# Kernel optimization log

Measured on AMD Instinct MI355X. Metric: run time of the kernel, lower is better.

The kernel has to match this reference:

```python
import jax, jax.numpy as jnp
import numpy as np

GAMMA_EXP = 1.0 / 2.2
PATTERN = 'RGGB'
H, W = 3072, 4096


def _conv1d(x, k, axis):
    """Cross-correlation of 2D x with 1D kernel k along axis, reflect padding
    (matches torch F.conv2d on reflect-padded input)."""
    p = (len(k) - 1) // 2
    pad = [(p, p) if a == axis else (0, 0) for a in range(2)]
    xp = jnp.pad(x, pad, mode='reflect')
    n = x.shape[axis]
    out = jnp.zeros_like(x)
    for i, ki in enumerate(k):
        if ki == 0.0:
            continue
        sl = [slice(None), slice(None)]
        sl[axis] = slice(i, i + n)
        out = out + ki * xp[tuple(sl)]
    return out


def _bayer_masks(shape, pattern):
    ch = {c: np.zeros((2, 2), np.float32) for c in 'RGB'}
    for i, c in enumerate(pattern):
        ch[c][i // 2, i % 2] = 1.0
    reps = ((shape[0] + 1) // 2, (shape[1] + 1) // 2)
    return tuple(jnp.asarray(np.tile(ch[c], reps)[:shape[0], :shape[1]]) for c in 'RGB')


def _shift_left2(x, axis):
    # pad by 2 on the far side with reflect, then drop first 2 -> x[j+2] with reflect at border
    pad = [(0, 2) if a == axis else (0, 0) for a in range(2)]
    xp = jnp.pad(x, pad, mode='reflect')
    sl = [slice(None), slice(None)]
    sl[axis] = slice(2, None)
    return xp[tuple(sl)]


def _menon2007(CFA, pattern):
    R_m, G_m, B_m = _bayer_masks(CFA.shape, pattern)
    h0 = [0.0, 0.5, 0.0, 0.5, 0.0]
    h1 = [-0.25, 0.0, 0.5, 0.0, -0.25]

    R = CFA * R_m
    G = CFA * G_m
    B = CFA * B_m

    G_H = jnp.where(G_m == 0, _conv1d(CFA, h0, 1) + _conv1d(CFA, h1, 1), G)
    G_V = jnp.where(G_m == 0, _conv1d(CFA, h0, 0) + _conv1d(CFA, h1, 0), G)

    C_H = jnp.where(R_m == 1, R - G_H, 0.0)
    C_H = jnp.where(B_m == 1, B - G_H, C_H)
    C_V = jnp.where(R_m == 1, R - G_V, 0.0)
    C_V = jnp.where(B_m == 1, B - G_V, C_V)

    D_H = jnp.abs(C_H - _shift_left2(C_H, axis=1))
    D_V = jnp.abs(C_V - _shift_left2(C_V, axis=0))

    k_row = [0.0, 0.0, 3.0, 0.0, 3.0]   # k[2, :]
    k_col = [1.0, 0.0, 3.0, 0.0, 1.0]   # k[:, 2]
    d_H = _conv1d(D_H, k_row, 1) + _conv1d(D_H, k_col, 0) - D_H * 3.0
    d_V = _conv1d(D_V, k_row, 1) + _conv1d(D_V, k_col, 0) - D_V * 3.0

    M = (d_V >= d_H).astype(CFA.dtype)
    G = jnp.where(G_m == 1, G, M * G_H + (1.0 - M) * G_V)

    R_r = jnp.any(R_m == 1, axis=1, keepdims=True) & jnp.ones_like(R_m, bool)
    B_r = jnp.any(B_m == 1, axis=1, keepdims=True) & jnp.ones_like(B_m, bool)
    kb = [0.5, 0.0, 0.5]

    R = jnp.where((G_m == 1) & R_r, G + _conv1d(R, kb, 1) - _conv1d(G, kb, 1), R)
    R = jnp.where((G_m == 1) & B_r, G + _conv1d(R, kb, 0) - _conv1d(G, kb, 0), R)
    B = jnp.where((G_m == 1) & B_r, G + _conv1d(B, kb, 1) - _conv1d(G, kb, 1), B)
    B = jnp.where((G_m == 1) & R_r, G + _conv1d(B, kb, 0) - _conv1d(G, kb, 0), B)

    R_at_B = M * (B + _conv1d(R, kb, 1) - _conv1d(B, kb, 1)) \
           + (1.0 - M) * (B + _conv1d(R, kb, 0) - _conv1d(B, kb, 0))
    R = jnp.where(B_r & (B_m == 1), R_at_B, R)

    B_at_R = M * (R + _conv1d(B, kb, 1) - _conv1d(R, kb, 1)) \
           + (1.0 - M) * (R + _conv1d(B, kb, 0) - _conv1d(R, kb, 0))
    B = jnp.where(R_r & (R_m == 1), B_at_R, B)

    return jnp.stack([R, G, B], axis=0)


def setup_inputs() -> dict:
    key = jax.random.key(0)
    k1, _ = jax.random.split(key)
    raw = jax.random.uniform(k1, (H, W), dtype=jnp.float32)
    wb = jnp.array([1.6, 1.2, 1.4], dtype=jnp.float32).reshape(3, 1, 1)
    return {"raw": raw, "wb": wb}


def reference(raw, wb):
    scaled = raw.astype(jnp.float32) / 65535.0
    rgb = _menon2007(scaled, PATTERN)
    rgb = rgb * wb
    rgb = jnp.clip(rgb, 0.0, 1.0)
    mn = jnp.min(rgb)
    mx = jnp.max(rgb)
    rng = mx - mn
    rgb = jnp.where(rng > 1e-6, (rgb - mn) / jnp.maximum(rng, 1e-12), rgb)
    rgb = jnp.power(jnp.maximum(rgb, 1e-12), GAMMA_EXP)
    return rgb
```

## Files before the change

kernel.cpp:

```cpp
#include <hip/hip_runtime.h>
#include <hip/hip_bf16.h>
#include <hip/hip_fp16.h>

#pragma clang fp contract(off)

constexpr int IMG_H = 3072;
constexpr int IMG_W = 4096;
constexpr int TS = 32;
constexpr float GAMMA_E = (float)(1.0 / 2.2);
constexpr float SC = 1048576.0f;
constexpr float INV_SC = 1.0f / SC;

__device__ __forceinline__ int mir(int v, int n) {
    v = (v < 0) ? -v : v;
    return (v >= n) ? (2 * n - 2 - v) : v;
}

constexpr int OFF_CFA = 0;               constexpr int CFA_STR = 45;
constexpr int OFF_GH  = OFF_CFA + 46*45; constexpr int GH_STR  = 41;
constexpr int OFF_GV  = OFF_GH  + 40*41; constexpr int GV_STR  = 39;
constexpr int OFF_DH  = OFF_GV  + 42*39; constexpr int DH_STR  = 39;
constexpr int OFF_DV  = OFF_DH  + 40*39; constexpr int DV_STR  = 39;
constexpr int OFF_G   = OFF_DV  + 40*39; constexpr int G_STR   = 37;
constexpr int SMEM_N  = OFF_G   + 36*37;
constexpr int OFF_HH  = OFF_DH;          constexpr int HV_STR  = 35;
constexpr int OFF_VV  = OFF_DV;

__global__ void init_slots(unsigned int* slots) {
    int t = threadIdx.x;
    if (t < 512) slots[t] = (t < 256) ? 0x7F800000u : 0u;
}

__device__ __forceinline__ float pack_gm(float g, unsigned mb) {
    return __uint_as_float((__float_as_uint(g) & ~1u) | mb);
}

template <bool FP16>
__global__ __launch_bounds__(256) void demosaic_pass1(
    const float* __restrict__ raw, const float* __restrict__ wb,
    float* __restrict__ out, __half* __restrict__ hout,
    unsigned int* __restrict__ slots)
{
    __shared__ float sm[SMEM_N];
    __shared__ float redmn[4], redmx[4];
    const int tid = threadIdx.x;
    const int tx = tid & 31, ty = tid >> 5;
    const int gr0 = blockIdx.y * TS;
    const int gc0 = blockIdx.x * TS;
    const bool fast = (blockIdx.x != 0) && (blockIdx.x != gridDim.x - 1) &&
                      (blockIdx.y != 0) && (blockIdx.y != gridDim.y - 1);

    if (fast) {
        const float* src = raw + (long long)(gr0 - 6) * IMG_W + (gc0 - 4);
        for (int i = tid; i < 46 * 11; i += 256) {
            int ar = i / 11, ic = (i % 11) << 2;
            float4 v = *(const float4*)(src + ar * IMG_W + ic);
            int b = OFF_CFA + ar * CFA_STR + ic;
            sm[b + 0] = v.x / 65535.0f; sm[b + 1] = v.y / 65535.0f;
            sm[b + 2] = v.z / 65535.0f; sm[b + 3] = v.w / 65535.0f;
        }
        __syncthreads();

        auto doGH = [&](int ar, int ac) {
            int cb = OFF_CFA + (ar + 2) * CFA_STR + (ac + 2);
            float x0 = sm[cb];
            float t0 = 0.5f * sm[cb - 1] + 0.5f * sm[cb + 1];
            float t1 = (-0.25f * sm[cb - 2] + 0.5f * x0) + (-0.25f * sm[cb + 2]);
            sm[OFF_GH + ar * GH_STR + ac] = ((ar + ac) & 1) ? x0 : (t0 + t1);
        };
        auto doGV = [&](int ar, int ac) {
            int cb = OFF_CFA + (ar + 2) * CFA_STR + (ac + 2);
            float x0 = sm[cb];
            float t0 = 0.5f * sm[cb - CFA_STR] + 0.5f * sm[cb + CFA_STR];
            float t1 = (-0.25f * sm[cb - 2 * CFA_STR] + 0.5f * x0) + (-0.25f * sm[cb + 2 * CFA_STR]);
            sm[OFF_GV + ar * GV_STR + ac] = ((ar + ac) & 1) ? x0 : (t0 + t1);
        };
#pragma unroll
        for (int r0 = 0; r0 < 5; ++r0) {
            int ar = ty + r0 * 8;
            doGH(ar, tx);
            if (tx < 8) doGH(ar, tx + 32);
        }
#pragma unroll
        for (int r0 = 0; r0 < 6; ++r0) {
            int ar = ty + r0 * 8;
            if (ar < 42) {
                doGV(ar, tx);
                if (tx < 6) doGV(ar, tx + 32);
            }
        }
        __syncthreads();

        auto doD = [&](int ar, int ac) {
            int cb = OFF_CFA + (ar + 2) * CFA_STR + (ac + 2);
            float c00 = sm[cb];
            float aH = c00 - sm[OFF_GH + ar * GH_STR + ac];
            float bH = sm[cb + 2] - sm[OFF_GH + ar * GH_STR + (ac + 2)];
            float aV = c00 - sm[OFF_GV + ar * GV_STR + ac];
            float bV = sm[cb + 2 * CFA_STR] - sm[OFF_GV + (ar + 2) * GV_STR + ac];
            sm[OFF_DH + ar * DH_STR + ac] = fabsf(aH - bH);
            sm[OFF_DV + ar * DV_STR + ac] = fabsf(aV - bV);
        };
#pragma unroll
        for (int r0 = 0; r0 < 5; ++r0) {
            int ar = ty + r0 * 8;
            doD(ar, tx);
            if (tx < 6) doD(ar, tx + 32);
        }
        __syncthreads();

        auto doMG = [&](int ar, int ac) {
            int db = OFF_DH + (ar + 2) * DH_STR + ac;
            float Dh0 = sm[db];
            float trowH = 3.0f * Dh0 + 3.0f * sm[db + 2];
            float tcolH = (sm[db - 2 * DH_STR] + 3.0f * Dh0) + sm[db + 2 * DH_STR];
            float dHv = (trowH + tcolH) - 3.0f * Dh0;
            int vb = OFF_DV + (ar + 2) * DV_STR + ac;
            float Dv0 = sm[vb];
            float trowV = 3.0f * Dv0 + 3.0f * sm[vb + 2];
            float tcolV = (sm[vb - 2 * DV_STR] + 3.0f * Dv0) + sm[vb + 2 * DV_STR];
            float dVv = (trowV + tcolV) - 3.0f * Dv0;
            unsigned mb = (dVv >= dHv) ? 1u : 0u;
            float g = ((ar + ac) & 1) ? sm[OFF_CFA + (ar + 4) * CFA_STR + (ac + 2)]
                     : (mb ? sm[OFF_GH + (ar + 2) * GH_STR + ac]
                           : sm[OFF_GV + (ar + 2) * GV_STR + ac]);
            sm[OFF_G + ar * G_STR + ac] = pack_gm(g, mb);
        };
#pragma unroll
        for (int r0 = 0; r0 < 5; ++r0) {
            int ar = ty + r0 * 8;
            if (ar < 36) {
                doMG(ar, tx);
                if (tx < 4) doMG(ar, tx + 32);
            }
        }
        __syncthreads();

        auto doHV = [&](int ar, int ac) {
            int gb = OFF_G + (ar + 1) * G_STR + (ac + 1);
            int cb = OFF_CFA + (ar + 5) * CFA_STR + (ac + 3);
            float g0 = sm[gb];
            float hh = g0 + 0.5f * (sm[cb - 1] + sm[cb + 1] - sm[gb - 1] - sm[gb + 1]);
            float vv = g0 + 0.5f * (sm[cb - CFA_STR] + sm[cb + CFA_STR] - sm[gb - G_STR] - sm[gb + G_STR]);
            sm[OFF_HH + ar * HV_STR + ac] = hh;
            sm[OFF_VV + ar * HV_STR + ac] = vv;
        };
#pragma unroll
        for (int r0 = 0; r0 < 5; ++r0) {
            int ar = ty + r0 * 8;
            if (ar < 34) {
                doHV(ar, tx);
                if (tx < 2) doHV(ar, tx + 32);
            }
        }
    } else {
        auto CFA = [&](int r, int c) -> float { return sm[OFF_CFA + (r - gr0 + 6) * CFA_STR + (c - gc0 + 4)]; };
        auto GH  = [&](int r, int c) -> float { return sm[OFF_GH  + (r - gr0 + 4) * GH_STR  + (c - gc0 + 2)]; };
        auto GV  = [&](int r, int c) -> float { return sm[OFF_GV  + (r - gr0 + 4) * GV_STR  + (c - gc0 + 2)]; };
        auto DH  = [&](int r, int c) -> float { return sm[OFF_DH  + (r - gr0 + 4) * DH_STR  + (c - gc0 + 2)]; };
        auto DV  = [&](int r, int c) -> float { return sm[OFF_DV  + (r - gr0 + 4) * DV_STR  + (c - gc0 + 2)]; };
        auto Gg  = [&](int r, int c) -> float { return sm[OFF_G   + (r - gr0 + 2) * G_STR   + (c - gc0 + 2)]; };

        for (int i = tid; i < 46 * 44; i += 256) {
            int ar = i / 44, ac = i % 44;
            int r2 = mir(gr0 + ar - 6, IMG_H), c2 = mir(gc0 + ac - 4, IMG_W);
            sm[OFF_CFA + ar * CFA_STR + ac] = raw[r2 * IMG_W + c2] / 65535.0f;
        }
        __syncthreads();
        for (int i = tid; i < 40 * 40; i += 256) {
            int ar = i / 40, ac = i % 40;
            int r2 = mir(gr0 + ar - 4, IMG_H), c2 = mir(gc0 + ac - 2, IMG_W);
            float x0 = CFA(r2, c2);
            float t0 = 0.5f * CFA(r2, c2 - 1) + 0.5f * CFA(r2, c2 + 1);
            float t1 = (-0.25f * CFA(r2, c2 - 2) + 0.5f * x0) + (-0.25f * CFA(r2, c2 + 2));
            sm[OFF_GH + ar * GH_STR + ac] = (((r2 + c2) & 1) ? x0 : (t0 + t1));
        }
        for (int i = tid; i < 42 * 38; i += 256) {
            int ar = i / 38, ac = i % 38;
            int r2 = mir(gr0 + ar - 4, IMG_H), c2 = mir(gc0 + ac - 2, IMG_W);
            float x0 = CFA(r2, c2);
            float t0 = 0.5f * CFA(r2 - 1, c2) + 0.5f * CFA(r2 + 1, c2);
            float t1 = (-0.25f * CFA(r2 - 2, c2) + 0.5f * x0) + (-0.25f * CFA(r2 + 2, c2));
            sm[OFF_GV + ar * GV_STR + ac] = (((r2 + c2) & 1) ? x0 : (t0 + t1));
        }
        __syncthreads();
        for (int i = tid; i < 40 * 38; i += 256) {
            int ar = i / 38, ac = i % 38;
            int r2 = mir(gr0 + ar - 4, IMG_H), c2 = mir(gc0 + ac - 2, IMG_W);
            float aH = CFA(r2, c2) - GH(r2, c2);
            float bH = CFA(r2, c2 + 2) - GH(r2, c2 + 2);
            float aV = CFA(r2, c2) - GV(r2, c2);
            float bV = CFA(r2 + 2, c2) - GV(r2 + 2, c2);
            sm[OFF_DH + ar * DH_STR + ac] = fabsf(aH - bH);
            sm[OFF_DV + ar * DV_STR + ac] = fabsf(aV - bV);
        }
        __syncthreads();
        for (int i = tid; i < 36 * 36; i += 256) {
            int ar = i / 36, ac = i % 36;
            int r2 = mir(gr0 + ar - 2, IMG_H), c2 = mir(gc0 + ac - 2, IMG_W);
            float Dh0 = DH(r2, c2);
            float trowH = 3.0f * Dh0 + 3.0f * DH(r2, c2 + 2);
            float tcolH = (DH(r2 - 2, c2) + 3.0f * Dh0) + DH(r2 + 2, c2);
            float dHv = (trowH + tcolH) - 3.0f * Dh0;
            float Dv0 = DV(r2, c2);
            float trowV = 3.0f * Dv0 + 3.0f * DV(r2, c2 + 2);
            float tcolV = (DV(r2 - 2, c2) + 3.0f * Dv0) + DV(r2 + 2, c2);
            float dVv = (trowV + tcolV) - 3.0f * Dv0;
            unsigned mb = (dVv >= dHv) ? 1u : 0u;
            float g = ((r2 + c2) & 1) ? CFA(r2, c2) : (mb ? GH(r2, c2) : GV(r2, c2));
            sm[OFF_G + ar * G_STR + ac] = pack_gm(g, mb);
        }
        __syncthreads();
        for (int i = tid; i < 34 * 34; i += 256) {
            int ar = i / 34, ac = i % 34;
            int r2 = mir(gr0 + ar - 1, IMG_H), c2 = mir(gc0 + ac - 1, IMG_W);
            float g0 = Gg(r2, c2);
            float hh = g0 + 0.5f * (CFA(r2, c2 - 1) + CFA(r2, c2 + 1) - Gg(r2, c2 - 1) - Gg(r2, c2 + 1));
            float vv = g0 + 0.5f * (CFA(r2 - 1, c2) + CFA(r2 + 1, c2) - Gg(r2 - 1, c2) - Gg(r2 + 1, c2));
            sm[OFF_HH + ar * HV_STR + ac] = hh;
            sm[OFF_VV + ar * HV_STR + ac] = vv;
        }
    }
    __syncthreads();

    const float wr = wb[0], wg = wb[1], wbv = wb[2];
    const int pr = tid >> 3;
    const int pc0 = (tid & 7) << 2;
    const bool rowOdd = (pr & 1) != 0;
    float mn = 1e30f, mx = -1e30f;
    float rr[4], gg[4], bb[4];
    __half hr[4], hg[4], hb[4];
#pragma unroll
    for (int d = 0; d < 4; ++d) {
        const int pc = pc0 + d;
        const int hhb = OFF_HH + (pr + 1) * HV_STR + (pc + 1);
        const int vvb = OFF_VV + (pr + 1) * HV_STR + (pc + 1);
        const float cfa = sm[OFF_CFA + (pr + 6) * CFA_STR + (pc + 4)];
        const float g = sm[OFF_G + (pr + 2) * G_STR + (pc + 2)];
        const unsigned mb = __float_as_uint(g) & 1u;
        float sH = (sm[hhb - 1] - sm[vvb - 1]) + (sm[hhb + 1] - sm[vvb + 1]);
        float sV = (sm[hhb - HV_STR] - sm[vvb - HV_STR]) + (sm[hhb + HV_STR] - sm[vvb + HV_STR]);
        float X = mb ? (cfa - 0.5f * sH) : (cfa + 0.5f * sV);
        float R, B;
        if ((d & 1) == 0) {
            R = rowOdd ? sm[vvb] : cfa;
            B = rowOdd ? sm[hhb] : X;
        } else {
            R = rowOdd ? X : sm[hhb];
            B = rowOdd ? cfa : sm[vvb];
        }
        R = fminf(fmaxf(R * wr, 0.f), 1.f);
        float Gx = fminf(fmaxf(g * wg, 0.f), 1.f);
        B = fminf(fmaxf(B * wbv, 0.f), 1.f);
        if constexpr (FP16) {
            hr[d] = __float2half(R * SC);  R  = __half2float(hr[d]);
            hg[d] = __float2half(Gx * SC); Gx = __half2float(hg[d]);
            hb[d] = __float2half(B * SC);  B  = __half2float(hb[d]);
        }
        mn = fminf(mn, fminf(R, fminf(Gx, B)));
        mx = fmaxf(mx, fmaxf(R, fmaxf(Gx, B)));
        rr[d] = R; gg[d] = Gx; bb[d] = B;
    }
    const long long HW = (long long)IMG_H * IMG_W;
    const long long base = (long long)(gr0 + pr) * IMG_W + (gc0 + pc0);
    if constexpr (FP16) {
        auto pack = [](__half a, __half b) {
            __half2 p = __halves2half2(a, b);
            return *reinterpret_cast<unsigned int*>(&p);
        };
        uint2 ur = make_uint2(pack(hr[0], hr[1]), pack(hr[2], hr[3]));
        uint2 ug = make_uint2(pack(hg[0], hg[1]), pack(hg[2], hg[3]));
        uint2 ub = make_uint2(pack(hb[0], hb[1]), pack(hb[2], hb[3]));
        *(uint2*)(hout + base)          = ur;
        *(uint2*)(hout + HW + base)     = ug;
        *(uint2*)(hout + 2 * HW + base) = ub;
    } else {
        *(float4*)(out + base)          = make_float4(rr[0], rr[1], rr[2], rr[3]);
        *(float4*)(out + HW + base)     = make_float4(gg[0], gg[1], gg[2], gg[3]);
        *(float4*)(out + 2 * HW + base) = make_float4(bb[0], bb[1], bb[2], bb[3]);
    }

#pragma unroll
    for (int off2 = 32; off2 > 0; off2 >>= 1) {
        mn = fminf(mn, __shfl_xor(mn, off2));
        mx = fmaxf(mx, __shfl_xor(mx, off2));
    }
    if ((tid & 63) == 0) { redmn[tid >> 6] = mn; redmx[tid >> 6] = mx; }
    __syncthreads();
    if (tid == 0) {
        mn = fminf(fminf(redmn[0], redmn[1]), fminf(redmn[2], redmn[3]));
        mx = fmaxf(fmaxf(redmx[0], redmx[1]), fmaxf(redmx[2], redmx[3]));
        if constexpr (FP16) { mn *= INV_SC; mx *= INV_SC; }
        int slot = (int)((blockIdx.y * gridDim.x + blockIdx.x) & 255);
        atomicMin(&slots[slot], __float_as_uint(mn));
        atomicMax(&slots[256 + slot], __float_as_uint(mx));
    }
}

__device__ __forceinline__ void reduce_slots(const unsigned int* slots, int tid,
                                             float* smn, float* smx, float& mn, float& mx) {
    mn = __uint_as_float(slots[tid]);
    mx = __uint_as_float(slots[256 + tid]);
#pragma unroll
    for (int off2 = 32; off2 > 0; off2 >>= 1) {
        mn = fminf(mn, __shfl_xor(mn, off2));
        mx = fmaxf(mx, __shfl_xor(mx, off2));
    }
    if ((tid & 63) == 0) { smn[tid >> 6] = mn; smx[tid >> 6] = mx; }
    __syncthreads();
    mn = fminf(fminf(smn[0], smn[1]), fminf(smn[2], smn[3]));
    mx = fmaxf(fmaxf(smx[0], smx[1]), fmaxf(smx[2], smx[3]));
}

__device__ __forceinline__ float gamma_hw(float a) {
    return __builtin_amdgcn_exp2f(GAMMA_E * __builtin_amdgcn_logf(a));
}

__global__ __launch_bounds__(256) void finalize_pass2_h(
    const __half* __restrict__ hin, float* __restrict__ out,
    const unsigned int* __restrict__ slots)
{
    __shared__ float smn[4], smx[4];
    const int tid = threadIdx.x;
    float mn, mx;
    reduce_slots(slots, tid, smn, smx, mn, mx);
    const float rng = mx - mn;
    const bool app = rng > 1e-6f;
    const float invden = 1.0f / fmaxf(rng, 1e-12f);

    const long long n8 = (long long)3 * IMG_H * IMG_W / 8;
    const uint4* pin = (const uint4*)hin;
    float4* po = (float4*)out;
    for (long long idx = (long long)blockIdx.x * blockDim.x + tid; idx < n8;
         idx += (long long)gridDim.x * blockDim.x) {
        uint4 u = pin[idx];
        float f[8];
        float2 t;
        t = __half22float2(*(__half2*)&u.x); f[0] = t.x; f[1] = t.y;
        t = __half22float2(*(__half2*)&u.y); f[2] = t.x; f[3] = t.y;
        t = __half22float2(*(__half2*)&u.z); f[4] = t.x; f[5] = t.y;
        t = __half22float2(*(__half2*)&u.w); f[6] = t.x; f[7] = t.y;
#pragma unroll
        for (int k = 0; k < 8; ++k) {
            float a = f[k] * INV_SC;
            a = app ? (a - mn) * invden : a;
            f[k] = gamma_hw(fmaxf(a, 1e-12f));
        }
        po[2 * idx]     = make_float4(f[0], f[1], f[2], f[3]);
        po[2 * idx + 1] = make_float4(f[4], f[5], f[6], f[7]);
    }
}

__global__ __launch_bounds__(256) void finalize_pass2_f(
    float* __restrict__ out, const unsigned int* __restrict__ slots)
{
    __shared__ float smn[4], smx[4];
    const int tid = threadIdx.x;
    float mn, mx;
    reduce_slots(slots, tid, smn, smx, mn, mx);
    const float rng = mx - mn;
    const bool app = rng > 1e-6f;
    const float invden = 1.0f / fmaxf(rng, 1e-12f);

    const long long n4 = (long long)3 * IMG_H * IMG_W / 4;
    float4* p = (float4*)out;
    for (long long idx = (long long)blockIdx.x * blockDim.x + tid; idx < n4;
         idx += (long long)gridDim.x * blockDim.x) {
        float4 v = p[idx];
        v.x = gamma_hw(fmaxf(app ? (v.x - mn) * invden : v.x, 1e-12f));
        v.y = gamma_hw(fmaxf(app ? (v.y - mn) * invden : v.y, 1e-12f));
        v.z = gamma_hw(fmaxf(app ? (v.z - mn) * invden : v.z, 1e-12f));
        v.w = gamma_hw(fmaxf(app ? (v.w - mn) * invden : v.w, 1e-12f));
        p[idx] = v;
    }
}

extern "C" void kernel_launch(void* const* d_in, const int* in_sizes, int n_in,
                              void* d_out, int out_size, void* d_ws, size_t ws_size,
                              hipStream_t stream) {
    (void)in_sizes; (void)n_in; (void)out_size;
    const float* raw = (const float*)d_in[0];
    const float* wb = (const float*)d_in[1];
    float* out = (float*)d_out;
    unsigned int* slots = (unsigned int*)d_ws;
    __half* hplanes = (__half*)((char*)d_ws + 4096);
    const size_t need = 4096 + (size_t)3 * IMG_H * IMG_W * sizeof(__half);
    const bool use_fp16 = ws_size >= need;

    init_slots<<<1, 512, 0, stream>>>(slots);
    dim3 grid(IMG_W / TS, IMG_H / TS);
    if (use_fp16) {
        demosaic_pass1<true><<<grid, 256, 0, stream>>>(raw, wb, out, hplanes, slots);
        finalize_pass2_h<<<dim3(2048), 256, 0, stream>>>(hplanes, out, slots);
    } else {
        demosaic_pass1<false><<<grid, 256, 0, stream>>>(raw, wb, out, hplanes, slots);
        finalize_pass2_f<<<dim3(2048), 256, 0, stream>>>(out, slots);
    }
}
```

Baseline: 170.6 us.

## Vectorize shared-memory stencil stages with aligned strides and float4 register windows

Changes all shared-memory tile strides to multiples of four and aligns the buffer. Each thread now processes four adjacent outputs per stage, loading sliding windows with float4/float2 LDS accesses and reusing them in registers, both in the interior fast path and the final output stage. This cuts LDS instruction count but gives up the odd padding strides, so bank conflicts may return and register pressure rises; the GV stage uses column-blocked register tiles.

Result: faster. 165.4 us (-3.1%).

```diff
diff --git a/kernel.cpp b/kernel.cpp
--- a/kernel.cpp
+++ b/kernel.cpp
@@ -16,14 +16,16 @@
     return (v >= n) ? (2 * n - 2 - v) : v;
 }
 
-constexpr int OFF_CFA = 0;               constexpr int CFA_STR = 45;
-constexpr int OFF_GH  = OFF_CFA + 46*45; constexpr int GH_STR  = 41;
-constexpr int OFF_GV  = OFF_GH  + 40*41; constexpr int GV_STR  = 39;
-constexpr int OFF_DH  = OFF_GV  + 42*39; constexpr int DH_STR  = 39;
-constexpr int OFF_DV  = OFF_DH  + 40*39; constexpr int DV_STR  = 39;
-constexpr int OFF_G   = OFF_DV  + 40*39; constexpr int G_STR   = 37;
-constexpr int SMEM_N  = OFF_G   + 36*37;
-constexpr int OFF_HH  = OFF_DH;          constexpr int HV_STR  = 35;
+constexpr int CFA_STR = 44, GH_STR = 40, GV_STR = 40, DH_STR = 40, DV_STR = 40,
+              G_STR = 36, HV_STR = 36;
+constexpr int OFF_CFA = 0;
+constexpr int OFF_GH  = OFF_CFA + 46*44;
+constexpr int OFF_GV  = OFF_GH  + 40*40;
+constexpr int OFF_DH  = OFF_GV  + 42*40;
+constexpr int OFF_DV  = OFF_DH  + 40*40;
+constexpr int OFF_G   = OFF_DV  + 40*40;
+constexpr int SMEM_N  = OFF_G   + 36*36;
+constexpr int OFF_HH  = OFF_DH;
 constexpr int OFF_VV  = OFF_DV;
 
 __global__ void init_slots(unsigned int* slots) {
@@ -41,10 +43,9 @@
     float* __restrict__ out, __half* __restrict__ hout,
     unsigned int* __restrict__ slots)
 {
-    __shared__ float sm[SMEM_N];
+    __shared__ __align__(16) float sm[SMEM_N];
     __shared__ float redmn[4], redmx[4];
     const int tid = threadIdx.x;
-    const int tx = tid & 31, ty = tid >> 5;
     const int gr0 = blockIdx.y * TS;
     const int gc0 = blockIdx.x * TS;
     const bool fast = (blockIdx.x != 0) && (blockIdx.x != gridDim.x - 1) &&
@@ -55,103 +56,161 @@
         for (int i = tid; i < 46 * 11; i += 256) {
             int ar = i / 11, ic = (i % 11) << 2;
             float4 v = *(const float4*)(src + ar * IMG_W + ic);
-            int b = OFF_CFA + ar * CFA_STR + ic;
-            sm[b + 0] = v.x / 65535.0f; sm[b + 1] = v.y / 65535.0f;
-            sm[b + 2] = v.z / 65535.0f; sm[b + 3] = v.w / 65535.0f;
-        }
-        __syncthreads();
-
-        auto doGH = [&](int ar, int ac) {
-            int cb = OFF_CFA + (ar + 2) * CFA_STR + (ac + 2);
-            float x0 = sm[cb];
-            float t0 = 0.5f * sm[cb - 1] + 0.5f * sm[cb + 1];
-            float t1 = (-0.25f * sm[cb - 2] + 0.5f * x0) + (-0.25f * sm[cb + 2]);
-            sm[OFF_GH + ar * GH_STR + ac] = ((ar + ac) & 1) ? x0 : (t0 + t1);
-        };
-        auto doGV = [&](int ar, int ac) {
-            int cb = OFF_CFA + (ar + 2) * CFA_STR + (ac + 2);
-            float x0 = sm[cb];
-            float t0 = 0.5f * sm[cb - CFA_STR] + 0.5f * sm[cb + CFA_STR];
-            float t1 = (-0.25f * sm[cb - 2 * CFA_STR] + 0.5f * x0) + (-0.25f * sm[cb + 2 * CFA_STR]);
-            sm[OFF_GV + ar * GV_STR + ac] = ((ar + ac) & 1) ? x0 : (t0 + t1);
-        };
-#pragma unroll
-        for (int r0 = 0; r0 < 5; ++r0) {
-            int ar = ty + r0 * 8;
-            doGH(ar, tx);
-            if (tx < 8) doGH(ar, tx + 32);
-        }
-#pragma unroll
-        for (int r0 = 0; r0 < 6; ++r0) {
-            int ar = ty + r0 * 8;
-            if (ar < 42) {
-                doGV(ar, tx);
-                if (tx < 6) doGV(ar, tx + 32);
-            }
-        }
-        __syncthreads();
-
-        auto doD = [&](int ar, int ac) {
-            int cb = OFF_CFA + (ar + 2) * CFA_STR + (ac + 2);
-            float c00 = sm[cb];
-            float aH = c00 - sm[OFF_GH + ar * GH_STR + ac];
-            float bH = sm[cb + 2] - sm[OFF_GH + ar * GH_STR + (ac + 2)];
-            float aV = c00 - sm[OFF_GV + ar * GV_STR + ac];
-            float bV = sm[cb + 2 * CFA_STR] - sm[OFF_GV + (ar + 2) * GV_STR + ac];
-            sm[OFF_DH + ar * DH_STR + ac] = fabsf(aH - bH);
-            sm[OFF_DV + ar * DV_STR + ac] = fabsf(aV - bV);
-        };
-#pragma unroll
-        for (int r0 = 0; r0 < 5; ++r0) {
-            int ar = ty + r0 * 8;
-            doD(ar, tx);
-            if (tx < 6) doD(ar, tx + 32);
-        }
-        __syncthreads();
-
-        auto doMG = [&](int ar, int ac) {
-            int db = OFF_DH + (ar + 2) * DH_STR + ac;
-            float Dh0 = sm[db];
-            float trowH = 3.0f * Dh0 + 3.0f * sm[db + 2];
-            float tcolH = (sm[db - 2 * DH_STR] + 3.0f * Dh0) + sm[db + 2 * DH_STR];
-            float dHv = (trowH + tcolH) - 3.0f * Dh0;
-            int vb = OFF_DV + (ar + 2) * DV_STR + ac;
-            float Dv0 = sm[vb];
-            float trowV = 3.0f * Dv0 + 3.0f * sm[vb + 2];
-            float tcolV = (sm[vb - 2 * DV_STR] + 3.0f * Dv0) + sm[vb + 2 * DV_STR];
-            float dVv = (trowV + tcolV) - 3.0f * Dv0;
-            unsigned mb = (dVv >= dHv) ? 1u : 0u;
-            float g = ((ar + ac) & 1) ? sm[OFF_CFA + (ar + 4) * CFA_STR + (ac + 2)]
-                     : (mb ? sm[OFF_GH + (ar + 2) * GH_STR + ac]
-                           : sm[OFF_GV + (ar + 2) * GV_STR + ac]);
-            sm[OFF_G + ar * G_STR + ac] = pack_gm(g, mb);
-        };
-#pragma unroll
-        for (int r0 = 0; r0 < 5; ++r0) {
-            int ar = ty + r0 * 8;
-            if (ar < 36) {
-                doMG(ar, tx);
-                if (tx < 4) doMG(ar, tx + 32);
-            }
-        }
-        __syncthreads();
-
-        auto doHV = [&](int ar, int ac) {
-            int gb = OFF_G + (ar + 1) * G_STR + (ac + 1);
-            int cb = OFF_CFA + (ar + 5) * CFA_STR + (ac + 3);
-            float g0 = sm[gb];
-            float hh = g0 + 0.5f * (sm[cb - 1] + sm[cb + 1] - sm[gb - 1] - sm[gb + 1]);
-            float vv = g0 + 0.5f * (sm[cb - CFA_STR] + sm[cb + CFA_STR] - sm[gb - G_STR] - sm[gb + G_STR]);
-            sm[OFF_HH + ar * HV_STR + ac] = hh;
-            sm[OFF_VV + ar * HV_STR + ac] = vv;
-        };
-#pragma unroll
-        for (int r0 = 0; r0 < 5; ++r0) {
-            int ar = ty + r0 * 8;
-            if (ar < 34) {
-                doHV(ar, tx);
-                if (tx < 2) doHV(ar, tx + 32);
-            }
+            *(float4*)&sm[OFF_CFA + ar * CFA_STR + ic] =
+                make_float4(v.x / 65535.0f, v.y / 65535.0f, v.z / 65535.0f, v.w / 65535.0f);
+        }
+        __syncthreads();
+
+        for (int i = tid; i < 400; i += 256) {
+            int ar = i / 10, ac4 = (i % 10) << 2;
+            int cb = OFF_CFA + (ar + 2) * CFA_STR + ac4;
+            const float4 a = *(const float4*)&sm[cb];
+            const float4 b = *(const float4*)&sm[cb + 4];
+            float w[8] = {a.x, a.y, a.z, a.w, b.x, b.y, b.z, b.w};
+            float o[4];
+#pragma unroll
+            for (int j = 0; j < 4; ++j) {
+                float x0 = w[j + 2];
+                float t0 = 0.5f * w[j + 1] + 0.5f * w[j + 3];
+                float t1 = (-0.25f * w[j] + 0.5f * x0) + (-0.25f * w[j + 4]);
+                o[j] = ((ar + ac4 + j) & 1) ? x0 : (t0 + t1);
+            }
+            *(float4*)&sm[OFF_GH + ar * GH_STR + ac4] = make_float4(o[0], o[1], o[2], o[3]);
+        }
+        if (tid < 110) {
+            int rg = tid / 10, ac4 = (tid % 10) << 2;
+            int r0 = (rg == 10) ? 38 : (rg << 2);
+            float c[4][8];
+#pragma unroll
+            for (int k = 0; k < 8; ++k) {
+                int rb = OFF_CFA + (r0 + k) * CFA_STR + ac4;
+                float2 p = *(const float2*)&sm[rb + 2];
+                float2 q = *(const float2*)&sm[rb + 4];
+                c[0][k] = p.x; c[1][k] = p.y; c[2][k] = q.x; c[3][k] = q.y;
+            }
+#pragma unroll
+            for (int ii = 0; ii < 4; ++ii) {
+                float o[4];
+#pragma unroll
+                for (int j = 0; j < 4; ++j) {
+                    float x0 = c[j][ii + 2];
+                    float t0 = 0.5f * c[j][ii + 1] + 0.5f * c[j][ii + 3];
+                    float t1 = (-0.25f * c[j][ii] + 0.5f * x0) + (-0.25f * c[j][ii + 4]);
+                    o[j] = ((r0 + ii + ac4 + j) & 1) ? x0 : (t0 + t1);
+                }
+                *(float4*)&sm[OFF_GV + (r0 + ii) * GV_STR + ac4] = make_float4(o[0], o[1], o[2], o[3]);
+            }
+        }
+        __syncthreads();
+
+        for (int i = tid; i < 400; i += 256) {
+            int ar = i / 10, ac4 = (i % 10) << 2;
+            int cb = OFF_CFA + (ar + 2) * CFA_STR + ac4;
+            const float4 a = *(const float4*)&sm[cb];
+            const float4 b = *(const float4*)&sm[cb + 4];
+            float cw[8] = {a.x, a.y, a.z, a.w, b.x, b.y, b.z, b.w};
+            float2 d0 = *(const float2*)&sm[OFF_CFA + (ar + 4) * CFA_STR + ac4 + 2];
+            float2 d1 = *(const float2*)&sm[OFF_CFA + (ar + 4) * CFA_STR + ac4 + 4];
+            float cd[4] = {d0.x, d0.y, d1.x, d1.y};
+            const float4 g0 = *(const float4*)&sm[OFF_GH + ar * GH_STR + ac4];
+            const float4 g1 = *(const float4*)&sm[OFF_GH + ar * GH_STR + ac4 + 4];
+            float gh[8] = {g0.x, g0.y, g0.z, g0.w, g1.x, g1.y, g1.z, g1.w};
+            const float4 v0 = *(const float4*)&sm[OFF_GV + ar * GV_STR + ac4];
+            const float4 v2 = *(const float4*)&sm[OFF_GV + (ar + 2) * GV_STR + ac4];
+            float gva[4] = {v0.x, v0.y, v0.z, v0.w};
+            float gvb[4] = {v2.x, v2.y, v2.z, v2.w};
+            float oh[4], ov[4];
+#pragma unroll
+            for (int j = 0; j < 4; ++j) {
+                float aH = cw[j + 2] - gh[j];
+                float bH = cw[j + 4] - gh[j + 2];
+                oh[j] = fabsf(aH - bH);
+                float aV = cw[j + 2] - gva[j];
+                float bV = cd[j] - gvb[j];
+                ov[j] = fabsf(aV - bV);
+            }
+            *(float4*)&sm[OFF_DH + ar * DH_STR + ac4] = make_float4(oh[0], oh[1], oh[2], oh[3]);
+            *(float4*)&sm[OFF_DV + ar * DV_STR + ac4] = make_float4(ov[0], ov[1], ov[2], ov[3]);
+        }
+        __syncthreads();
+
+        for (int i = tid; i < 324; i += 256) {
+            int ar = i / 9, ac4 = (i % 9) << 2;
+            int hb2 = OFF_DH + (ar + 2) * DH_STR + ac4;
+            const float4 h0 = *(const float4*)&sm[hb2];
+            const float4 h1 = *(const float4*)&sm[hb2 + 4];
+            float hw[8] = {h0.x, h0.y, h0.z, h0.w, h1.x, h1.y, h1.z, h1.w};
+            const float4 huq = *(const float4*)&sm[OFF_DH + ar * DH_STR + ac4];
+            const float4 hdq = *(const float4*)&sm[OFF_DH + (ar + 4) * DH_STR + ac4];
+            float hu[4] = {huq.x, huq.y, huq.z, huq.w};
+            float hd[4] = {hdq.x, hdq.y, hdq.z, hdq.w};
+            int vb2 = OFF_DV + (ar + 2) * DV_STR + ac4;
+            const float4 w0 = *(const float4*)&sm[vb2];
+            const float4 w1 = *(const float4*)&sm[vb2 + 4];
+            float vw[8] = {w0.x, w0.y, w0.z, w0.w, w1.x, w1.y, w1.z, w1.w};
+            const float4 vuq = *(const float4*)&sm[OFF_DV + ar * DV_STR + ac4];
+            const float4 vdq = *(const float4*)&sm[OFF_DV + (ar + 4) * DV_STR + ac4];
+            float vu[4] = {vuq.x, vuq.y, vuq.z, vuq.w};
+            float vd[4] = {vdq.x, vdq.y, vdq.z, vdq.w};
+            float2 c0 = *(const float2*)&sm[OFF_CFA + (ar + 4) * CFA_STR + ac4 + 2];
+            float2 c1 = *(const float2*)&sm[OFF_CFA + (ar + 4) * CFA_STR + ac4 + 4];
+            float cf[4] = {c0.x, c0.y, c1.x, c1.y};
+            const float4 ghq = *(const float4*)&sm[OFF_GH + (ar + 2) * GH_STR + ac4];
+            const float4 gvq = *(const float4*)&sm[OFF_GV + (ar + 2) * GV_STR + ac4];
+            float gha[4] = {ghq.x, ghq.y, ghq.z, ghq.w};
+            float gvv[4] = {gvq.x, gvq.y, gvq.z, gvq.w};
+            float o[4];
+#pragma unroll
+            for (int j = 0; j < 4; ++j) {
+                float Dh0 = hw[j];
+                float trowH = 3.0f * Dh0 + 3.0f * hw[j + 2];
+                float tcolH = (hu[j] + 3.0f * Dh0) + hd[j];
+                float dHv = (trowH + tcolH) - 3.0f * Dh0;
+                float Dv0 = vw[j];
+                float trowV = 3.0f * Dv0 + 3.0f * vw[j + 2];
+                float tcolV = (vu[j] + 3.0f * Dv0) + vd[j];
+                float dVv = (trowV + tcolV) - 3.0f * Dv0;
+                unsigned mb = (dVv >= dHv) ? 1u : 0u;
+                float g = ((ar + ac4 + j) & 1) ? cf[j] : (mb ? gha[j] : gvv[j]);
+                o[j] = pack_gm(g, mb);
+            }
+            *(float4*)&sm[OFF_G + ar * G_STR + ac4] = make_float4(o[0], o[1], o[2], o[3]);
+        }
+        __syncthreads();
+
+        for (int i = tid; i < 306; i += 256) {
+            int ar = i / 9, ac4 = (i % 9) << 2;
+            int gb1 = OFF_G + (ar + 1) * G_STR + ac4;
+            const float4 ga = *(const float4*)&sm[gb1];
+            const float4 gb2 = *(const float4*)&sm[gb1 + 4];
+            float gw[8] = {ga.x, ga.y, ga.z, ga.w, gb2.x, gb2.y, gb2.z, gb2.w};
+            const float4 guq = *(const float4*)&sm[OFF_G + ar * G_STR + ac4];
+            const float2 guq2 = *(const float2*)&sm[OFF_G + ar * G_STR + ac4 + 4];
+            float gu[6] = {guq.x, guq.y, guq.z, guq.w, guq2.x, guq2.y};
+            const float4 gdq = *(const float4*)&sm[OFF_G + (ar + 2) * G_STR + ac4];
+            const float2 gdq2 = *(const float2*)&sm[OFF_G + (ar + 2) * G_STR + ac4 + 4];
+            float gd[6] = {gdq.x, gdq.y, gdq.z, gdq.w, gdq2.x, gdq2.y};
+            int c5 = OFF_CFA + (ar + 5) * CFA_STR + ac4;
+            const float4 ca = *(const float4*)&sm[c5];
+            const float4 cb2 = *(const float4*)&sm[c5 + 4];
+            float cw[8] = {ca.x, ca.y, ca.z, ca.w, cb2.x, cb2.y, cb2.z, cb2.w};
+            int c4i = OFF_CFA + (ar + 4) * CFA_STR + ac4;
+            const float4 cua = *(const float4*)&sm[c4i];
+            const float4 cub = *(const float4*)&sm[c4i + 4];
+            float cu[8] = {cua.x, cua.y, cua.z, cua.w, cub.x, cub.y, cub.z, cub.w};
+            int c6i = OFF_CFA + (ar + 6) * CFA_STR + ac4;
+            const float4 cda = *(const float4*)&sm[c6i];
+            const float4 cdb = *(const float4*)&sm[c6i + 4];
+            float cdn[8] = {cda.x, cda.y, cda.z, cda.w, cdb.x, cdb.y, cdb.z, cdb.w};
+            float oh[4], ov[4];
+#pragma unroll
+            for (int j = 0; j < 4; ++j) {
+                float g0 = gw[j + 1];
+                oh[j] = g0 + 0.5f * (cw[j + 2] + cw[j + 4] - gw[j] - gw[j + 2]);
+                ov[j] = g0 + 0.5f * (cu[j + 3] + cdn[j + 3] - gu[j + 1] - gd[j + 1]);
+            }
+            *(float4*)&sm[OFF_HH + ar * HV_STR + ac4] = make_float4(oh[0], oh[1], oh[2], oh[3]);
+            *(float4*)&sm[OFF_VV + ar * HV_STR + ac4] = make_float4(ov[0], ov[1], ov[2], ov[3]);
         }
     } else {
         auto CFA = [&](int r, int c) -> float { return sm[OFF_CFA + (r - gr0 + 6) * CFA_STR + (c - gc0 + 4)]; };
@@ -227,39 +286,62 @@
     const int pr = tid >> 3;
     const int pc0 = (tid & 7) << 2;
     const bool rowOdd = (pr & 1) != 0;
+    int hbase = OFF_HH + (pr + 1) * HV_STR + pc0;
+    const float4 h1a = *(const float4*)&sm[hbase];
+    const float4 h1b = *(const float4*)&sm[hbase + 4];
+    float hwc[8] = {h1a.x, h1a.y, h1a.z, h1a.w, h1b.x, h1b.y, h1b.z, h1b.w};
+    int vbase = OFF_VV + (pr + 1) * HV_STR + pc0;
+    const float4 v1a = *(const float4*)&sm[vbase];
+    const float4 v1b = *(const float4*)&sm[vbase + 4];
+    float vwc[8] = {v1a.x, v1a.y, v1a.z, v1a.w, v1b.x, v1b.y, v1b.z, v1b.w};
+    const float4 huq = *(const float4*)&sm[OFF_HH + pr * HV_STR + pc0];
+    const float2 huq2 = *(const float2*)&sm[OFF_HH + pr * HV_STR + pc0 + 4];
+    float hu[6] = {huq.x, huq.y, huq.z, huq.w, huq2.x, huq2.y};
+    const float4 hdq = *(const float4*)&sm[OFF_HH + (pr + 2) * HV_STR + pc0];
+    const float2 hdq2 = *(const float2*)&sm[OFF_HH + (pr + 2) * HV_STR + pc0 + 4];
+    float hd[6] = {hdq.x, hdq.y, hdq.z, hdq.w, hdq2.x, hdq2.y};
+    const float4 vuq = *(const float4*)&sm[OFF_VV + pr * HV_STR + pc0];
+    const float2 vuq2 = *(const float2*)&sm[OFF_VV + pr * HV_STR + pc0 + 4];
+    float vu[6] = {vuq.x, vuq.y, vuq.z, vuq.w, vuq2.x, vuq2.y};
+    const float4 vdq = *(const float4*)&sm[OFF_VV + (pr + 2) * HV_STR + pc0];
+    const float2 vdq2 = *(const float2*)&sm[OFF_VV + (pr + 2) * HV_STR + pc0 + 4];
+    float vd[6] = {vdq.x, vdq.y, vdq.z, vdq.w, vdq2.x, vdq2.y};
+    const float4 cfq = *(const float4*)&sm[OFF_CFA + (pr + 6) * CFA_STR + pc0 + 4];
+    float cf[4] = {cfq.x, cfq.y, cfq.z, cfq.w};
+    const float2 gq0 = *(const float2*)&sm[OFF_G + (pr + 2) * G_STR + pc0 + 2];
+    const float2 gq1 = *(const float2*)&sm[OFF_G + (pr + 2) * G_STR + pc0 + 4];
+    float ggr[4] = {gq0.x, gq0.y, gq1.x, gq1.y};
+
     float mn = 1e30f, mx = -1e30f;
-    float rr[4], gg[4], bb[4];
-    __half hr[4], hg[4], hb[4];
-#pragma unroll
-    for (int d = 0; d < 4; ++d) {
-        const int pc = pc0 + d;
-        const int hhb = OFF_HH + (pr + 1) * HV_STR + (pc + 1);
-        const int vvb = OFF_VV + (pr + 1) * HV_STR + (pc + 1);
-        const float cfa = sm[OFF_CFA + (pr + 6) * CFA_STR + (pc + 4)];
-        const float g = sm[OFF_G + (pr + 2) * G_STR + (pc + 2)];
+    float rr[4], go[4], bo[4];
+    __half hR[4], hG[4], hB[4];
+#pragma unroll
+    for (int j = 0; j < 4; ++j) {
+        const float cfa = cf[j];
+        const float g = ggr[j];
         const unsigned mb = __float_as_uint(g) & 1u;
-        float sH = (sm[hhb - 1] - sm[vvb - 1]) + (sm[hhb + 1] - sm[vvb + 1]);
-        float sV = (sm[hhb - HV_STR] - sm[vvb - HV_STR]) + (sm[hhb + HV_STR] - sm[vvb + HV_STR]);
+        float sH = (hwc[j] - vwc[j]) + (hwc[j + 2] - vwc[j + 2]);
+        float sV = (hu[j + 1] - vu[j + 1]) + (hd[j + 1] - vd[j + 1]);
         float X = mb ? (cfa - 0.5f * sH) : (cfa + 0.5f * sV);
         float R, B;
-        if ((d & 1) == 0) {
-            R = rowOdd ? sm[vvb] : cfa;
-            B = rowOdd ? sm[hhb] : X;
+        if ((j & 1) == 0) {
+            R = rowOdd ? vwc[j + 1] : cfa;
+            B = rowOdd ? hwc[j + 1] : X;
         } else {
-            R = rowOdd ? X : sm[hhb];
-            B = rowOdd ? cfa : sm[vvb];
+            R = rowOdd ? X : hwc[j + 1];
+            B = rowOdd ? cfa : vwc[j + 1];
         }
         R = fminf(fmaxf(R * wr, 0.f), 1.f);
         float Gx = fminf(fmaxf(g * wg, 0.f), 1.f);
         B = fminf(fmaxf(B * wbv, 0.f), 1.f);
         if constexpr (FP16) {
-            hr[d] = __float2half(R * SC);  R  = __half2float(hr[d]);
-            hg[d] = __float2half(Gx * SC); Gx = __half2float(hg[d]);
-            hb[d] = __float2half(B * SC);  B  = __half2float(hb[d]);
+            hR[j] = __float2half(R * SC);  R  = __half2float(hR[j]);
+            hG[j] = __float2half(Gx * SC); Gx = __half2float(hG[j]);
+            hB[j] = __float2half(B * SC);  B  = __half2float(hB[j]);
         }
         mn = fminf(mn, fminf(R, fminf(Gx, B)));
         mx = fmaxf(mx, fmaxf(R, fmaxf(Gx, B)));
-        rr[d] = R; gg[d] = Gx; bb[d] = B;
+        rr[j] = R; go[j] = Gx; bo[j] = B;
     }
     const long long HW = (long long)IMG_H * IMG_W;
     const long long base = (long long)(gr0 + pr) * IMG_W + (gc0 + pc0);
@@ -268,16 +350,13 @@
             __half2 p = __halves2half2(a, b);
             return *reinterpret_cast<unsigned int*>(&p);
         };
-        uint2 ur = make_uint2(pack(hr[0], hr[1]), pack(hr[2], hr[3]));
-        uint2 ug = make_uint2(pack(hg[0], hg[1]), pack(hg[2], hg[3]));
-        uint2 ub = make_uint2(pack(hb[0], hb[1]), pack(hb[2], hb[3]));
-        *(uint2*)(hout + base)          = ur;
-        *(uint2*)(hout + HW + base)     = ug;
-        *(uint2*)(hout + 2 * HW + base) = ub;
+        *(uint2*)(hout + base)          = make_uint2(pack(hR[0], hR[1]), pack(hR[2], hR[3]));
+        *(uint2*)(hout + HW + base)     = make_uint2(pack(hG[0], hG[1]), pack(hG[2], hG[3]));
+        *(uint2*)(hout + 2 * HW + base) = make_uint2(pack(hB[0], hB[1]), pack(hB[2], hB[3]));
     } else {
         *(float4*)(out + base)          = make_float4(rr[0], rr[1], rr[2], rr[3]);
-        *(float4*)(out + HW + base)     = make_float4(gg[0], gg[1], gg[2], gg[3]);
-        *(float4*)(out + 2 * HW + base) = make_float4(bb[0], bb[1], bb[2], bb[3]);
+        *(float4*)(out + HW + base)     = make_float4(go[0], go[1], go[2], go[3]);
+        *(float4*)(out + 2 * HW + base) = make_float4(bo[0], bo[1], bo[2], bo[3]);
     }
 
 #pragma unroll
```
